# Kernel tuning notes

Hardware: AMD Instinct MI355X
Metric: run time of the kernel (lower is better)

The kernel has to match this reference:

```python
import jax, jax.numpy as jnp
import numpy as np

N, D, K = 131072, 64, 1024


def setup_inputs() -> dict:
    key = jax.random.key(0)
    kx, kc = jax.random.split(key)
    x = jax.random.normal(kx, (N, D), dtype=jnp.float32)
    codebook = jax.random.normal(kc, (K, D), dtype=jnp.float32)
    return {"x": x, "codebook": codebook}


def reference(x, codebook):
    # Pairwise squared L2 distances, expanded form to avoid the [N, K, D]
    # intermediate the naive vmap would materialize:
    x_sq = jnp.sum(x * x, axis=-1, keepdims=True)            # [N, 1]
    c_sq = jnp.sum(codebook * codebook, axis=-1)             # [K]
    xc = jnp.einsum("nd,kd->nk", x, codebook)                # [N, K]
    l2_sum = x_sq - 2.0 * xc + c_sq[None, :]                 # [N, K]
    codes = jnp.argmin(l2_sum, axis=-1)                      # [N] int
    code_vec = jnp.take(codebook, codes, axis=0)             # [N, D]
    return (code_vec, codes, l2_sum)
```

## Files before the change

kernel.cpp:

```cpp
#include <hip/hip_runtime.h>
#include <stdint.h>

#define NROWS 131072
#define DDIM  64
#define KCB   1024
#define BM    128
#define NCHUNK 16
#define XPAD  68

typedef short bf16x8 __attribute__((ext_vector_type(8)));
typedef float f32x4  __attribute__((ext_vector_type(4)));

__device__ __forceinline__ unsigned short f2bf(float f) {
    unsigned int u = __float_as_uint(f);
    u += 0x7FFFu + ((u >> 16) & 1u);
    return (unsigned short)(u >> 16);
}
__device__ __forceinline__ float bf2f(unsigned short h) {
    return __uint_as_float(((unsigned int)h) << 16);
}

__global__ __launch_bounds__(256)
void convert_cb(const float* __restrict__ cb,
                unsigned short* __restrict__ mh,
                unsigned short* __restrict__ ml,
                float* __restrict__ csq) {
    const int t    = blockIdx.x * 256 + threadIdx.x;
    const int row  = t >> 2;
    const int part = t & 3;
    const float4* src = (const float4*)(cb + (size_t)row * DDIM + part * 16);

    unsigned short hb[16], lb[16];
    float s = 0.f;
#pragma unroll
    for (int q = 0; q < 4; ++q) {
        float4 v = src[q];
        float c, m; unsigned short h;
        c = v.x; s = fmaf(c, c, s); m = -2.f * c; h = f2bf(m);
        hb[q*4+0] = h; lb[q*4+0] = f2bf(m - bf2f(h));
        c = v.y; s = fmaf(c, c, s); m = -2.f * c; h = f2bf(m);
        hb[q*4+1] = h; lb[q*4+1] = f2bf(m - bf2f(h));
        c = v.z; s = fmaf(c, c, s); m = -2.f * c; h = f2bf(m);
        hb[q*4+2] = h; lb[q*4+2] = f2bf(m - bf2f(h));
        c = v.w; s = fmaf(c, c, s); m = -2.f * c; h = f2bf(m);
        hb[q*4+3] = h; lb[q*4+3] = f2bf(m - bf2f(h));
    }
    s += __shfl_xor(s, 1);
    s += __shfl_xor(s, 2);
    if (part == 0) csq[row] = s;

    const size_t off = (size_t)row * DDIM + part * 16;
    short4* dh = (short4*)(mh + off);
    short4* dl = (short4*)(ml + off);
#pragma unroll
    for (int q = 0; q < 4; ++q) {
        short4 hv, lv;
        hv.x = (short)hb[q*4+0]; hv.y = (short)hb[q*4+1];
        hv.z = (short)hb[q*4+2]; hv.w = (short)hb[q*4+3];
        lv.x = (short)lb[q*4+0]; lv.y = (short)lb[q*4+1];
        lv.z = (short)lb[q*4+2]; lv.w = (short)lb[q*4+3];
        dh[q] = hv; dl[q] = lv;
    }
}

__device__ __forceinline__ void cvt8(float4 f0, float4 f1, bf16x8* h, bf16x8* l) {
    bf16x8 hh, ll;
    float fv; unsigned short hb;
    fv = f0.x; hb = f2bf(fv); hh[0] = (short)hb; ll[0] = (short)f2bf(fv - bf2f(hb));
    fv = f0.y; hb = f2bf(fv); hh[1] = (short)hb; ll[1] = (short)f2bf(fv - bf2f(hb));
    fv = f0.z; hb = f2bf(fv); hh[2] = (short)hb; ll[2] = (short)f2bf(fv - bf2f(hb));
    fv = f0.w; hb = f2bf(fv); hh[3] = (short)hb; ll[3] = (short)f2bf(fv - bf2f(hb));
    fv = f1.x; hb = f2bf(fv); hh[4] = (short)hb; ll[4] = (short)f2bf(fv - bf2f(hb));
    fv = f1.y; hb = f2bf(fv); hh[5] = (short)hb; ll[5] = (short)f2bf(fv - bf2f(hb));
    fv = f1.z; hb = f2bf(fv); hh[6] = (short)hb; ll[6] = (short)f2bf(fv - bf2f(hb));
    fv = f1.w; hb = f2bf(fv); hh[7] = (short)hb; ll[7] = (short)f2bf(fv - bf2f(hb));
    *h = hh; *l = ll;
}

__global__ __launch_bounds__(256, 3)
void codebook_mfma(const float* __restrict__ x,
                   const float* __restrict__ cb,
                   const unsigned short* __restrict__ cbh,
                   const unsigned short* __restrict__ cbl,
                   const float* __restrict__ csq,
                   float* __restrict__ out_codevec,
                   float* __restrict__ out_codes,
                   float* __restrict__ out_l2) {
    __shared__ float xs[BM][XPAD];
    __shared__ float tb[4][16][XPAD];
    __shared__ float xsq_s[BM];
    __shared__ int   cand_s[BM][2];

    const int tid  = threadIdx.x;
    const int lane = tid & 63;
    const int wid  = tid >> 6;
    const int row0 = blockIdx.x * BM;

    {
        const int r = tid >> 1, h = tid & 1;
        const float4* src = (const float4*)(x + (size_t)(row0 + r) * DDIM + h * 32);
        float4* dst = (float4*)&xs[r][h * 32];
        float s0 = 0.f, s1 = 0.f;
#pragma unroll
        for (int q = 0; q < 8; ++q) {
            float4 v = src[q];
            dst[q] = v;
            s0 = fmaf(v.x, v.x, s0); s0 = fmaf(v.y, v.y, s0);
            s1 = fmaf(v.z, v.z, s1); s1 = fmaf(v.w, v.w, s1);
        }
        float s = s0 + s1;
        s += __shfl_xor(s, 1);
        if (h == 0) xsq_s[r] = s;
    }
    __syncthreads();

    const int mrow = wid * 32;
    const int cl   = lane & 15;
    const int ch   = lane >> 4;

    bf16x8 ah[2][2], al[2][2];
#pragma unroll
    for (int mt = 0; mt < 2; ++mt)
#pragma unroll
    for (int ks = 0; ks < 2; ++ks) {
        const float* p = &xs[mrow + mt * 16 + cl][ks * 32 + ch * 8];
        cvt8(*(const float4*)p, *(const float4*)(p + 4), &ah[mt][ks], &al[mt][ks]);
    }

    float xq[2][4];
#pragma unroll
    for (int mt = 0; mt < 2; ++mt)
#pragma unroll
    for (int rg = 0; rg < 4; ++rg)
        xq[mt][rg] = xsq_s[mrow + mt * 16 + ch * 4 + rg];

    float m1[2][4], m2[2][4];
    int   i1[2][4], i2[2][4];
#pragma unroll
    for (int mt = 0; mt < 2; ++mt)
#pragma unroll
    for (int rg = 0; rg < 4; ++rg) {
        m1[mt][rg] = 3.4e38f; m2[mt][rg] = 3.4e38f;
        i1[mt][rg] = 0;       i2[mt][rg] = 0;
    }

    for (int chunk = 0; chunk < NCHUNK; ++chunk) {
        const int k0 = chunk << 6;

        bf16x8 vbh0[4], vbh1[4], vbl0[4], vbl1[4];
        float  cq[4];
#pragma unroll
        for (int nt = 0; nt < 4; ++nt) {
            const int ncol = k0 + nt * 16 + cl;
            const size_t bof = (size_t)ncol * DDIM + ch * 8;
            vbh0[nt] = *(const bf16x8*)(cbh + bof);
            vbh1[nt] = *(const bf16x8*)(cbh + bof + 32);
            vbl0[nt] = *(const bf16x8*)(cbl + bof);
            vbl1[nt] = *(const bf16x8*)(cbl + bof + 32);
            cq[nt]   = csq[ncol];
        }

#pragma unroll
        for (int mt = 0; mt < 2; ++mt) {
#pragma unroll
            for (int nt = 0; nt < 4; ++nt) {
                const int ncol = k0 + nt * 16 + cl;
                f32x4 a;
                a[0] = xq[mt][0] + cq[nt]; a[1] = xq[mt][1] + cq[nt];
                a[2] = xq[mt][2] + cq[nt]; a[3] = xq[mt][3] + cq[nt];
                a = __builtin_amdgcn_mfma_f32_16x16x32_bf16(ah[mt][0], vbh0[nt], a, 0, 0, 0);
                a = __builtin_amdgcn_mfma_f32_16x16x32_bf16(ah[mt][1], vbh1[nt], a, 0, 0, 0);
                a = __builtin_amdgcn_mfma_f32_16x16x32_bf16(ah[mt][0], vbl0[nt], a, 0, 0, 0);
                a = __builtin_amdgcn_mfma_f32_16x16x32_bf16(ah[mt][1], vbl1[nt], a, 0, 0, 0);
                a = __builtin_amdgcn_mfma_f32_16x16x32_bf16(al[mt][0], vbh0[nt], a, 0, 0, 0);
                a = __builtin_amdgcn_mfma_f32_16x16x32_bf16(al[mt][1], vbh1[nt], a, 0, 0, 0);
#pragma unroll
                for (int rg = 0; rg < 4; ++rg) {
                    const float l2 = a[rg];
                    tb[wid][ch * 4 + rg][nt * 16 + cl] = l2;
                    const bool c1 = l2 < m1[mt][rg];
                    const bool c2 = l2 < m2[mt][rg];
                    const float nm2 = c1 ? m1[mt][rg] : (c2 ? l2 : m2[mt][rg]);
                    const int   ni2 = c1 ? i1[mt][rg] : (c2 ? ncol : i2[mt][rg]);
                    m2[mt][rg] = nm2; i2[mt][rg] = ni2;
                    m1[mt][rg] = c1 ? l2 : m1[mt][rg];
                    i1[mt][rg] = c1 ? ncol : i1[mt][rg];
                }
            }
            asm volatile("s_waitcnt lgkmcnt(0)" ::: "memory");
#pragma unroll
            for (int s = 0; s < 4; ++s) {
                const f32x4 v = *(const f32x4*)&tb[wid][s * 4 + ch][cl * 4];
                f32x4* dst = (f32x4*)(out_l2 +
                    (size_t)(row0 + mrow + mt * 16 + s * 4 + ch) * KCB + k0 + cl * 4);
                __builtin_nontemporal_store(v, dst);
            }
        }
    }

#pragma unroll
    for (int mt = 0; mt < 2; ++mt)
#pragma unroll
    for (int rg = 0; rg < 4; ++rg) {
        float a1 = m1[mt][rg], a2 = m2[mt][rg];
        int   j1 = i1[mt][rg], j2 = i2[mt][rg];
#pragma unroll
        for (int mm = 1; mm < 16; mm <<= 1) {
            float o1 = __shfl_xor(a1, mm), o2 = __shfl_xor(a2, mm);
            int   q1 = __shfl_xor(j1, mm), q2 = __shfl_xor(j2, mm);
            const bool fw = (o1 < a1) || (o1 == a1 && q1 < j1);
            const float w1 = fw ? o1 : a1; const int wj1 = fw ? q1 : j1;
            const float ca = fw ? a1 : o1; const int cja = fw ? j1 : q1;
            const float cbv = fw ? o2 : a2; const int cjb = fw ? q2 : j2;
            const bool sw = (cbv < ca) || (cbv == ca && cjb < cja);
            a1 = w1; j1 = wj1;
            a2 = sw ? cbv : ca; j2 = sw ? cjb : cja;
        }
        if (cl == 0) {
            const int r = mrow + mt * 16 + ch * 4 + rg;
            cand_s[r][0] = j1; cand_s[r][1] = j2;
        }
    }
    __syncthreads();

    {
        const int r = tid >> 1, h = tid & 1;
        const int cand = cand_s[r][h];
        const float4* xr = (const float4*)&xs[r][0];
        const float4* cr = (const float4*)(cb + (size_t)cand * DDIM);
        float s0 = 0.f, s1 = 0.f, s2 = 0.f, s3 = 0.f;
#pragma unroll
        for (int q = 0; q < 4; ++q) {
            float4 xa, ca;
            xa = xr[q];      ca = cr[q];
            s0 = fmaf(xa.x, ca.x, s0); s0 = fmaf(xa.y, ca.y, s0);
            s0 = fmaf(xa.z, ca.z, s0); s0 = fmaf(xa.w, ca.w, s0);
            xa = xr[q + 4];  ca = cr[q + 4];
            s1 = fmaf(xa.x, ca.x, s1); s1 = fmaf(xa.y, ca.y, s1);
            s1 = fmaf(xa.z, ca.z, s1); s1 = fmaf(xa.w, ca.w, s1);
            xa = xr[q + 8];  ca = cr[q + 8];
            s2 = fmaf(xa.x, ca.x, s2); s2 = fmaf(xa.y, ca.y, s2);
            s2 = fmaf(xa.z, ca.z, s2); s2 = fmaf(xa.w, ca.w, s2);
            xa = xr[q + 12]; ca = cr[q + 12];
            s3 = fmaf(xa.x, ca.x, s3); s3 = fmaf(xa.y, ca.y, s3);
            s3 = fmaf(xa.z, ca.z, s3); s3 = fmaf(xa.w, ca.w, s3);
        }
        const float dot = (s0 + s1) + (s2 + s3);
        const float d = fmaf(-2.f, dot, xsq_s[r] + csq[cand]);
        const float od = __shfl_xor(d, 1);
        const int   oc = __shfl_xor(cand, 1);
        const bool win = (d < od) || (d == od && cand < oc);
        const int w = win ? cand : oc;
        if (h == 0) out_codes[row0 + r] = (float)w;
        const f32x4* wv = (const f32x4*)(cb + (size_t)w * DDIM + h * 32);
        f32x4* ov = (f32x4*)(out_codevec + (size_t)(row0 + r) * DDIM + h * 32);
#pragma unroll
        for (int q = 0; q < 8; ++q) __builtin_nontemporal_store(wv[q], ov + q);
    }
}

extern "C" void kernel_launch(void* const* d_in, const int* in_sizes, int n_in,
                              void* d_out, int out_size, void* d_ws, size_t ws_size,
                              hipStream_t stream) {
    (void)in_sizes; (void)n_in; (void)out_size; (void)ws_size;
    const float* x  = (const float*)d_in[0];
    const float* cb = (const float*)d_in[1];

    unsigned short* cbh = (unsigned short*)d_ws;
    unsigned short* cbl = cbh + (size_t)KCB * DDIM;
    float*          csq = (float*)(cbl + (size_t)KCB * DDIM);

    float* out_codevec = (float*)d_out;
    float* out_codes   = out_codevec + (size_t)NROWS * DDIM;
    float* out_l2      = out_codes + NROWS;

    convert_cb<<<16, 256, 0, stream>>>(cb, cbh, cbl, csq);
    codebook_mfma<<<NROWS / BM, 256, 0, stream>>>(x, cb, cbh, cbl, csq,
                                                  out_codevec, out_codes, out_l2);
}
```

Baseline: 237.5 us.

## Swap MFMA operands so lanes own rows, storing L2 directly without LDS transpose

Swaps the A/B operands of the bf16 MFMAs so that each lane's accumulator holds four consecutive codebook columns of a single x row. Each L2 tile can then be written to global memory straight from registers as a 16-byte nontemporal store, which removes the LDS transpose buffer, its waitcnt and the readback. The per-row argmin tracking drops from 8 to 2 running minima per lane, and the final cross-lane reduction needs only two shuffle steps instead of four. The global stores now cover 16-byte pieces spread across 16 different rows per instruction rather than contiguous runs within a row, which may hurt write coalescing.

```diff
diff --git a/kernel.cpp b/kernel.cpp
--- a/kernel.cpp
+++ b/kernel.cpp
@@ -87,7 +87,6 @@
                    float* __restrict__ out_codes,
                    float* __restrict__ out_l2) {
     __shared__ float xs[BM][XPAD];
-    __shared__ float tb[4][16][XPAD];
     __shared__ float xsq_s[BM];
     __shared__ int   cand_s[BM][2];
 
@@ -118,37 +117,31 @@
     const int cl   = lane & 15;
     const int ch   = lane >> 4;
 
-    bf16x8 ah[2][2], al[2][2];
+    bf16x8 xh[2][2], xl[2][2];
 #pragma unroll
     for (int mt = 0; mt < 2; ++mt)
 #pragma unroll
     for (int ks = 0; ks < 2; ++ks) {
         const float* p = &xs[mrow + mt * 16 + cl][ks * 32 + ch * 8];
-        cvt8(*(const float4*)p, *(const float4*)(p + 4), &ah[mt][ks], &al[mt][ks]);
-    }
-
-    float xq[2][4];
-#pragma unroll
-    for (int mt = 0; mt < 2; ++mt)
-#pragma unroll
-    for (int rg = 0; rg < 4; ++rg)
-        xq[mt][rg] = xsq_s[mrow + mt * 16 + ch * 4 + rg];
-
-    float m1[2][4], m2[2][4];
-    int   i1[2][4], i2[2][4];
-#pragma unroll
-    for (int mt = 0; mt < 2; ++mt)
-#pragma unroll
-    for (int rg = 0; rg < 4; ++rg) {
-        m1[mt][rg] = 3.4e38f; m2[mt][rg] = 3.4e38f;
-        i1[mt][rg] = 0;       i2[mt][rg] = 0;
+        cvt8(*(const float4*)p, *(const float4*)(p + 4), &xh[mt][ks], &xl[mt][ks]);
+    }
+
+    float xq[2];
+    xq[0] = xsq_s[mrow + cl];
+    xq[1] = xsq_s[mrow + 16 + cl];
+
+    float m1[2], m2[2];
+    int   i1[2], i2[2];
+#pragma unroll
+    for (int mt = 0; mt < 2; ++mt) {
+        m1[mt] = 3.4e38f; m2[mt] = 3.4e38f; i1[mt] = 0; i2[mt] = 0;
     }
 
     for (int chunk = 0; chunk < NCHUNK; ++chunk) {
         const int k0 = chunk << 6;
 
         bf16x8 vbh0[4], vbh1[4], vbl0[4], vbl1[4];
-        float  cq[4];
+        f32x4  cqv[4];
 #pragma unroll
         for (int nt = 0; nt < 4; ++nt) {
             const int ncol = k0 + nt * 16 + cl;
@@ -157,55 +150,50 @@
             vbh1[nt] = *(const bf16x8*)(cbh + bof + 32);
             vbl0[nt] = *(const bf16x8*)(cbl + bof);
             vbl1[nt] = *(const bf16x8*)(cbl + bof + 32);
-            cq[nt]   = csq[ncol];
+            cqv[nt]  = *(const f32x4*)(csq + k0 + nt * 16 + ch * 4);
         }
 
 #pragma unroll
         for (int mt = 0; mt < 2; ++mt) {
 #pragma unroll
             for (int nt = 0; nt < 4; ++nt) {
-                const int ncol = k0 + nt * 16 + cl;
                 f32x4 a;
-                a[0] = xq[mt][0] + cq[nt]; a[1] = xq[mt][1] + cq[nt];
-                a[2] = xq[mt][2] + cq[nt]; a[3] = xq[mt][3] + cq[nt];
-                a = __builtin_amdgcn_mfma_f32_16x16x32_bf16(ah[mt][0], vbh0[nt], a, 0, 0, 0);
-                a = __builtin_amdgcn_mfma_f32_16x16x32_bf16(ah[mt][1], vbh1[nt], a, 0, 0, 0);
-                a = __builtin_amdgcn_mfma_f32_16x16x32_bf16(ah[mt][0], vbl0[nt], a, 0, 0, 0);
-                a = __builtin_amdgcn_mfma_f32_16x16x32_bf16(ah[mt][1], vbl1[nt], a, 0, 0, 0);
-                a = __builtin_amdgcn_mfma_f32_16x16x32_bf16(al[mt][0], vbh0[nt], a, 0, 0, 0);
-                a = __builtin_amdgcn_mfma_f32_16x16x32_bf16(al[mt][1], vbh1[nt], a, 0, 0, 0);
+                a[0] = xq[mt] + cqv[nt][0]; a[1] = xq[mt] + cqv[nt][1];
+                a[2] = xq[mt] + cqv[nt][2]; a[3] = xq[mt] + cqv[nt][3];
+                a = __builtin_amdgcn_mfma_f32_16x16x32_bf16(vbh0[nt], xh[mt][0], a, 0, 0, 0);
+                a = __builtin_amdgcn_mfma_f32_16x16x32_bf16(vbh1[nt], xh[mt][1], a, 0, 0, 0);
+                a = __builtin_amdgcn_mfma_f32_16x16x32_bf16(vbh0[nt], xl[mt][0], a, 0, 0, 0);
+                a = __builtin_amdgcn_mfma_f32_16x16x32_bf16(vbh1[nt], xl[mt][1], a, 0, 0, 0);
+                a = __builtin_amdgcn_mfma_f32_16x16x32_bf16(vbl0[nt], xh[mt][0], a, 0, 0, 0);
+                a = __builtin_amdgcn_mfma_f32_16x16x32_bf16(vbl1[nt], xh[mt][1], a, 0, 0, 0);
+
+                f32x4* dst = (f32x4*)(out_l2 +
+                    (size_t)(row0 + mrow + mt * 16 + cl) * KCB + k0 + nt * 16 + ch * 4);
+                __builtin_nontemporal_store(a, dst);
+
+                const int idx0 = k0 + nt * 16 + ch * 4;
 #pragma unroll
                 for (int rg = 0; rg < 4; ++rg) {
-                    const float l2 = a[rg];
-                    tb[wid][ch * 4 + rg][nt * 16 + cl] = l2;
-                    const bool c1 = l2 < m1[mt][rg];
-                    const bool c2 = l2 < m2[mt][rg];
-                    const float nm2 = c1 ? m1[mt][rg] : (c2 ? l2 : m2[mt][rg]);
-                    const int   ni2 = c1 ? i1[mt][rg] : (c2 ? ncol : i2[mt][rg]);
-                    m2[mt][rg] = nm2; i2[mt][rg] = ni2;
-                    m1[mt][rg] = c1 ? l2 : m1[mt][rg];
-                    i1[mt][rg] = c1 ? ncol : i1[mt][rg];
+                    const float v = a[rg];
+                    const int idx = idx0 + rg;
+                    const bool c1 = v < m1[mt];
+                    const bool c2 = v < m2[mt];
+                    const float nm2 = c1 ? m1[mt] : (c2 ? v : m2[mt]);
+                    const int   ni2 = c1 ? i1[mt] : (c2 ? idx : i2[mt]);
+                    m2[mt] = nm2; i2[mt] = ni2;
+                    m1[mt] = c1 ? v : m1[mt];
+                    i1[mt] = c1 ? idx : i1[mt];
                 }
             }
-            asm volatile("s_waitcnt lgkmcnt(0)" ::: "memory");
-#pragma unroll
-            for (int s = 0; s < 4; ++s) {
-                const f32x4 v = *(const f32x4*)&tb[wid][s * 4 + ch][cl * 4];
-                f32x4* dst = (f32x4*)(out_l2 +
-                    (size_t)(row0 + mrow + mt * 16 + s * 4 + ch) * KCB + k0 + cl * 4);
-                __builtin_nontemporal_store(v, dst);
-            }
-        }
-    }
-
-#pragma unroll
-    for (int mt = 0; mt < 2; ++mt)
-#pragma unroll
-    for (int rg = 0; rg < 4; ++rg) {
-        float a1 = m1[mt][rg], a2 = m2[mt][rg];
-        int   j1 = i1[mt][rg], j2 = i2[mt][rg];
-#pragma unroll
-        for (int mm = 1; mm < 16; mm <<= 1) {
+        }
+    }
+
+#pragma unroll
+    for (int mt = 0; mt < 2; ++mt) {
+        float a1 = m1[mt], a2 = m2[mt];
+        int   j1 = i1[mt], j2 = i2[mt];
+#pragma unroll
+        for (int mm = 16; mm <= 32; mm <<= 1) {
             float o1 = __shfl_xor(a1, mm), o2 = __shfl_xor(a2, mm);
             int   q1 = __shfl_xor(j1, mm), q2 = __shfl_xor(j2, mm);
             const bool fw = (o1 < a1) || (o1 == a1 && q1 < j1);
@@ -216,8 +204,8 @@
             a1 = w1; j1 = wj1;
             a2 = sw ? cbv : ca; j2 = sw ? cjb : cja;
         }
-        if (cl == 0) {
-            const int r = mrow + mt * 16 + ch * 4 + rg;
+        if (ch == 0) {
+            const int r = mrow + mt * 16 + cl;
             cand_s[r][0] = j1; cand_s[r][1] = j2;
         }
     }
```

After: 274.5 us. 15.6% more time.
